# Performance work log

Measured on AMD Instinct MI355X. Metric: run time of the kernel, lower is better.

## Reference

```python
import jax, jax.numpy as jnp
import numpy as np

NUM_USERS = 100000
NUM_ITEMS = 50000
N = NUM_USERS + NUM_ITEMS  # total nodes
DIM = 64                   # dim_h
E = 2000000                # number of edges
NUM_LAYERS = 2


def setup_inputs() -> dict:
    key = jax.random.key(0)
    k0, k1, k2, k3, k4 = jax.random.split(key, 5)
    edge_index = jax.random.randint(k0, (2, E), 0, N, dtype=jnp.int64)
    edge_weight = jax.random.uniform(k1, (E,), dtype=jnp.float32)
    # nn.init.normal_(std=0.01) embeddings
    emb_users = 0.01 * jax.random.normal(k2, (NUM_USERS, DIM), dtype=jnp.float32)
    emb_items = 0.01 * jax.random.normal(k3, (NUM_ITEMS, DIM), dtype=jnp.float32)
    # nn.Linear(dim_h, dim_h)
    kW, kb = jax.random.split(k4)
    bound = 1.0 / np.sqrt(DIM)
    W = jax.random.uniform(kW, (DIM, DIM), minval=-bound, maxval=bound, dtype=jnp.float32)
    b = jax.random.uniform(kb, (DIM,), minval=-bound, maxval=bound, dtype=jnp.float32)
    return {"edge_index": edge_index, "edge_weight": edge_weight,
            "emb_users": emb_users, "emb_items": emb_items, "W": W, "b": b}


def reference(edge_index, edge_weight, emb_users, emb_items, W, b):
    # emb = cat([user_emb, item_emb])  -> [N, DIM]
    emb = jnp.concatenate([emb_users, emb_items], axis=0)
    src, dst = edge_index[0], edge_index[1]
    acc = emb  # running sum over layer embeddings (embs list)
    for _ in range(NUM_LAYERS):
        # LGConv with edge_weight: out[i] = sum_{j->i} w * x[j], then .relu()
        msg = edge_weight[:, None] * emb[src]            # [E, DIM] gather
        emb = jax.nn.relu(jax.ops.segment_sum(msg, dst, num_segments=N))
        acc = acc + emb
    emb_final = acc / (NUM_LAYERS + 1)                   # mean over stacked embs
    emb_final = emb_final @ W.T + b                      # final linear
    emb_users_final = emb_final[:NUM_USERS]
    emb_items_final = emb_final[NUM_USERS:]
    return (emb_users_final, emb_users, emb_items_final, emb_items)
```

## Files before the change

### kernel.cpp

```cpp
#include <hip/hip_runtime.h>
#include <hip/hip_fp16.h>

#define NUSERS 100000
#define NITEMS 50000
#define NNODES (NUSERS + NITEMS)
#define DIM 64
#define NEDGE 2000000
#define FT_ROWS 256
#define FT_BLOCKS ((NNODES + FT_ROWS - 1) / FT_ROWS)

#define BSH 7
#define NB ((NNODES + 127) >> BSH)
#define CAP 2048
#define CHUNK 4096
#define ABLOCKS ((NEDGE + CHUNK - 1) / CHUNK)
#define CONVB ((NNODES * DIM / 4 + 511) / 512)

__global__ __launch_bounds__(512)
void bucketconv_kernel(const int* __restrict__ eidx, const float* __restrict__ ew,
                       int* __restrict__ gcur, int2* __restrict__ regions,
                       const float* __restrict__ eu, const float* __restrict__ eit,
                       __half* __restrict__ tbl) {
    const int t = threadIdx.x;

    if (blockIdx.x >= ABLOCKS) {
        long i = (long)(blockIdx.x - ABLOCKS) * 512 + t;
        const long total = (long)NNODES * DIM / 4;
        if (i < total) {
            const long ue = (long)NUSERS * DIM / 4;
            float4 v = (i < ue) ? ((const float4*)eu)[i] : ((const float4*)eit)[i - ue];
            ((__half2*)tbl)[2 * i + 0] = __floats2half2_rn(v.x, v.y);
            ((__half2*)tbl)[2 * i + 1] = __floats2half2_rn(v.z, v.w);
        }
        return;
    }

    __shared__ int cursor_s[NB];
    __shared__ int excl_s[NB];
    __shared__ int gbase_s[NB];
    __shared__ int scanbuf[512];
    __shared__ int2 stage[CHUNK];
    __shared__ unsigned short sbkt[CHUNK];

    const int e0 = blockIdx.x * CHUNK;
    const int cnt_edges = min(CHUNK, NEDGE - e0);

    for (int i = t; i < NB; i += 512) cursor_s[i] = 0;
    __syncthreads();

    int2 recs[8];
    int bk[8];
    const int e4base = e0 >> 2;
#pragma unroll
    for (int k = 0; k < 2; ++k) {
        int g = k * 512 + t;
        bool ok = (4 * g) < cnt_edges;
        int4 s4 = make_int4(0, 0, 0, 0), d4 = make_int4(0, 0, 0, 0);
        float4 w4 = make_float4(0.f, 0.f, 0.f, 0.f);
        if (ok) {
            int e4 = e4base + g;
            s4 = ((const int4*)eidx)[e4];
            d4 = ((const int4*)eidx)[(NEDGE >> 2) + e4];
            w4 = ((const float4*)ew)[e4];
        }
        int ss[4] = {s4.x, s4.y, s4.z, s4.w};
        int dd[4] = {d4.x, d4.y, d4.z, d4.w};
        float ww[4] = {w4.x, w4.y, w4.z, w4.w};
#pragma unroll
        for (int j = 0; j < 4; ++j) {
            int idx = 4 * k + j;
            if (ok) {
                int d = dd[j];
                int b = d >> BSH;
                bk[idx] = b;
                recs[idx].x = ss[j] | ((d & 127) << 18);
                recs[idx].y = __float_as_int(ww[j]);
                atomicAdd(&cursor_s[b], 1);
            } else {
                bk[idx] = -1;
            }
        }
    }
    __syncthreads();

    int myv[3];
    int tsum = 0;
    const int base_i = t * 3;
#pragma unroll
    for (int j = 0; j < 3; ++j) {
        int i = base_i + j;
        myv[j] = (i < NB) ? cursor_s[i] : 0;
        tsum += myv[j];
    }
    scanbuf[t] = tsum;
    __syncthreads();
    for (int d = 1; d < 512; d <<= 1) {
        int u = (t >= d) ? scanbuf[t - d] : 0;
        __syncthreads();
        scanbuf[t] += u;
        __syncthreads();
    }
    int run = scanbuf[t] - tsum;
#pragma unroll
    for (int j = 0; j < 3; ++j) {
        int i = base_i + j;
        if (i < NB) {
            excl_s[i] = run;
            cursor_s[i] = run;
            if (myv[j] > 0) gbase_s[i] = atomicAdd(&gcur[i], myv[j]);
            run += myv[j];
        }
    }
    __syncthreads();

#pragma unroll
    for (int k = 0; k < 8; ++k) {
        if (bk[k] >= 0) {
            int p = atomicAdd(&cursor_s[bk[k]], 1);
            stage[p] = recs[k];
            sbkt[p] = (unsigned short)bk[k];
        }
    }
    __syncthreads();

    for (int i = t; i < cnt_edges; i += 512) {
        int b = sbkt[i];
        int gpos = gbase_s[b] + (i - excl_s[b]);
        if (gpos < CAP) regions[(long)b * CAP + gpos] = stage[i];
    }
}

__global__ __launch_bounds__(512)
void sortpull1_kernel(const int* __restrict__ gcur, const int2* __restrict__ regions,
                      const __half* __restrict__ tbl,
                      int2* __restrict__ edge_sorted, int2* __restrict__ rs,
                      __half* __restrict__ buf1h) {
    __shared__ int2 srec[CAP];
    __shared__ int cnt[128];
    __shared__ int excl[128];
    __shared__ int scanbuf[128];
    const int t = threadIdx.x;
    const int b = blockIdx.x;
    const int node0 = b << BSH;
    const int ecnt = min(gcur[b], CAP);
    const long gbase = (long)b * CAP;

    if (t < 128) cnt[t] = 0;
    __syncthreads();

    int2 recs[4];
#pragma unroll
    for (int k = 0; k < 4; ++k) {
        int i = k * 512 + t;
        if (i < ecnt) {
            recs[k] = regions[gbase + i];
            atomicAdd(&cnt[(recs[k].x >> 18) & 127], 1);
        }
    }
    __syncthreads();

    if (t < 128) scanbuf[t] = cnt[t];
    __syncthreads();
    for (int d = 1; d < 128; d <<= 1) {
        int u = 0;
        if (t < 128 && t >= d) u = scanbuf[t - d];
        __syncthreads();
        if (t < 128) scanbuf[t] += u;
        __syncthreads();
    }
    if (t < 128) {
        excl[t] = scanbuf[t] - cnt[t];
        cnt[t] = scanbuf[t] - cnt[t];
    }
    __syncthreads();

#pragma unroll
    for (int k = 0; k < 4; ++k) {
        int i = k * 512 + t;
        if (i < ecnt) {
            int d = (recs[k].x >> 18) & 127;
            int p = atomicAdd(&cnt[d], 1);
            int2 o;
            o.x = recs[k].x & 0x3FFFF;
            o.y = recs[k].y;
            srec[p] = o;
        }
    }
    __syncthreads();

    for (int i = t; i < ecnt; i += 512) edge_sorted[gbase + i] = srec[i];
    if (t < 128) {
        int node = node0 + t;
        if (node < NNODES) {
            int2 p;
            p.x = (int)gbase + excl[t];
            p.y = (int)gbase + cnt[t];
            rs[node] = p;
        }
    }

    const int lane = t & 63;
    const int wv = t >> 6;
    const int half = lane >> 5;
    const int hl = lane & 31;
    const __half2* tb2 = (const __half2*)tbl;
#pragma unroll 1
    for (int j = 0; j < 16; ++j) {
        const int local = wv * 16 + j;
        const int node = node0 + local;
        if (node >= NNODES) break;
        int i = excl[local];
        const int iend = cnt[local];
        float ax = 0.f, ay = 0.f, bx = 0.f, by = 0.f;
        for (; i + 7 < iend; i += 8) {
#pragma unroll
            for (int u = 0; u < 4; ++u) {
                int2 r = srec[i + 2 * u + half];
                float w = __int_as_float(r.y);
                float2 v = __half22float2(tb2[((long)r.x << 5) + hl]);
                if (u & 1) { bx = fmaf(w, v.x, bx); by = fmaf(w, v.y, by); }
                else       { ax = fmaf(w, v.x, ax); ay = fmaf(w, v.y, ay); }
            }
        }
        if (i < iend) {
#pragma unroll
            for (int u = 0; u < 4; ++u) {
                int idx = i + 2 * u + half;
                if (idx < iend) {
                    int2 r = srec[idx];
                    float w = __int_as_float(r.y);
                    float2 v = __half22float2(tb2[((long)r.x << 5) + hl]);
                    if (u & 1) { bx = fmaf(w, v.x, bx); by = fmaf(w, v.y, by); }
                    else       { ax = fmaf(w, v.x, ax); ay = fmaf(w, v.y, ay); }
                }
            }
        }
        float sx = ax + bx, sy = ay + by;
        sx += __shfl_xor(sx, 32);
        sy += __shfl_xor(sy, 32);
        if (half == 0) {
            ((__half2*)buf1h)[((long)node << 5) + hl] =
                __floats2half2_rn(fmaxf(sx, 0.f), fmaxf(sy, 0.f));
        }
    }
}

__global__ __launch_bounds__(512)
void pull2_kernel(const int* __restrict__ gcur, const int2* __restrict__ rs,
                  const int2* __restrict__ edge_sorted,
                  const __half* __restrict__ in_emb,
                  __half* __restrict__ out_emb) {
    __shared__ int2 srec[CAP];
    __shared__ int2 rsl[128];
    const int t = threadIdx.x;
    const int b = blockIdx.x;
    const int node0 = b << BSH;
    const int ecnt = min(gcur[b], CAP);
    const long gbase = (long)b * CAP;

    for (int i = t; i < ecnt; i += 512) srec[i] = edge_sorted[gbase + i];
    if (t < 128) {
        int node = node0 + t;
        rsl[t] = (node < NNODES) ? rs[node] : make_int2(0, 0);
    }
    __syncthreads();

    const int lane = t & 63;
    const int wv = t >> 6;
    const int half = lane >> 5;
    const int hl = lane & 31;
    const __half2* tb2 = (const __half2*)in_emb;
#pragma unroll 1
    for (int j = 0; j < 16; ++j) {
        const int local = wv * 16 + j;
        const int node = node0 + local;
        if (node >= NNODES) break;
        int i = rsl[local].x - (int)gbase;
        const int iend = rsl[local].y - (int)gbase;
        float ax = 0.f, ay = 0.f, bx = 0.f, by = 0.f;
        for (; i + 7 < iend; i += 8) {
#pragma unroll
            for (int u = 0; u < 4; ++u) {
                int2 r = srec[i + 2 * u + half];
                float w = __int_as_float(r.y);
                float2 v = __half22float2(tb2[((long)r.x << 5) + hl]);
                if (u & 1) { bx = fmaf(w, v.x, bx); by = fmaf(w, v.y, by); }
                else       { ax = fmaf(w, v.x, ax); ay = fmaf(w, v.y, ay); }
            }
        }
        if (i < iend) {
#pragma unroll
            for (int u = 0; u < 4; ++u) {
                int idx = i + 2 * u + half;
                if (idx < iend) {
                    int2 r = srec[idx];
                    float w = __int_as_float(r.y);
                    float2 v = __half22float2(tb2[((long)r.x << 5) + hl]);
                    if (u & 1) { bx = fmaf(w, v.x, bx); by = fmaf(w, v.y, by); }
                    else       { ax = fmaf(w, v.x, ax); ay = fmaf(w, v.y, ay); }
                }
            }
        }
        float sx = ax + bx, sy = ay + by;
        sx += __shfl_xor(sx, 32);
        sy += __shfl_xor(sy, 32);
        if (half == 0) {
            ((__half2*)out_emb)[((long)node << 5) + hl] =
                __floats2half2_rn(fmaxf(sx, 0.f), fmaxf(sy, 0.f));
        }
    }
}

__global__ __launch_bounds__(512)
void final_kernel(const float* __restrict__ eu, const float* __restrict__ eit,
                  const __half* __restrict__ e1, const __half* __restrict__ e2,
                  const float* __restrict__ W, const float* __restrict__ bias,
                  float* __restrict__ out) {
    __shared__ float4 As4[FT_ROWS * 16];
    __shared__ float Wt[64][64];
    const int t = threadIdx.x;
    const int lane = t & 63;
    const int wv = t >> 6;
    const long R0 = (long)blockIdx.x * FT_ROWS;

#pragma unroll
    for (int it = 0; it < 2; ++it) {
        int idx = it * 512 + t;
        int j = idx >> 4, q = idx & 15;
        float4 w = ((const float4*)W)[idx];
        Wt[4 * q + 0][j] = w.x; Wt[4 * q + 1][j] = w.y;
        Wt[4 * q + 2][j] = w.z; Wt[4 * q + 3][j] = w.w;
    }

#pragma unroll
    for (int it = 0; it < 8; ++it) {
        int idx = it * 512 + t;
        long row = R0 + (idx >> 4);
        if (row < NNODES) {
            int q = idx & 15;
            const float4* g0;
            long co;
            if (row < NUSERS) {
                g0 = (const float4*)(eu + (row << 6));
                co = (long)NUSERS * DIM + (row << 6);
            } else {
                g0 = (const float4*)(eit + ((row - NUSERS) << 6));
                co = (long)2 * NUSERS * DIM + (long)NITEMS * DIM + ((row - NUSERS) << 6);
            }
            float4 v0 = g0[q];
            ((float4*)(out + co))[q] = v0;
            const __half2* h1 = (const __half2*)(e1 + (row << 6));
            const __half2* h2 = (const __half2*)(e2 + (row << 6));
            float2 f1a = __half22float2(h1[2 * q]), f1b = __half22float2(h1[2 * q + 1]);
            float2 f2a = __half22float2(h2[2 * q]), f2b = __half22float2(h2[2 * q + 1]);
            float4 s;
            s.x = v0.x + f1a.x + f2a.x; s.y = v0.y + f1a.y + f2a.y;
            s.z = v0.z + f1b.x + f2b.x; s.w = v0.w + f1b.y + f2b.y;
            As4[idx] = s;
        }
    }
    __syncthreads();

    float wreg[64];
#pragma unroll
    for (int k = 0; k < 64; ++k) wreg[k] = Wt[k][lane];
    const float bj = bias[lane];

#pragma unroll 4
    for (int r = 0; r < 32; ++r) {
        int tr = wv * 32 + r;
        long row = R0 + tr;
        if (row >= NNODES) break;
        const float4* a = As4 + tr * 16;
        float s0 = 0.f, s1 = 0.f;
#pragma unroll
        for (int k = 0; k < 16; ++k) {
            float4 v = a[k];
            s0 = fmaf(v.x, wreg[4 * k + 0], s0);
            s1 = fmaf(v.y, wreg[4 * k + 1], s1);
            s0 = fmaf(v.z, wreg[4 * k + 2], s0);
            s1 = fmaf(v.w, wreg[4 * k + 3], s1);
        }
        float val = fmaf(s0 + s1, (1.0f / 3.0f), bj);
        long o = (row < NUSERS) ? row * DIM
                                : (long)2 * NUSERS * DIM + (row - NUSERS) * DIM;
        out[o + lane] = val;
    }
}

extern "C" void kernel_launch(void* const* d_in, const int* in_sizes, int n_in,
                              void* d_out, int out_size, void* d_ws, size_t ws_size,
                              hipStream_t stream) {
    const int*   eidx = (const int*)d_in[0];
    const float* ew   = (const float*)d_in[1];
    const float* eu   = (const float*)d_in[2];
    const float* eit  = (const float*)d_in[3];
    const float* W    = (const float*)d_in[4];
    const float* bias = (const float*)d_in[5];
    float* out = (float*)d_out;

    const size_t nfeat = (size_t)NNODES * DIM;
    __half* tbl         = (__half*)d_ws;
    __half* buf1h       = tbl + nfeat;
    __half* buf2h       = buf1h + nfeat;
    int2*   regions     = (int2*)(buf2h + nfeat);
    int2*   edge_sorted = regions + (long)NB * CAP;
    int2*   rs          = edge_sorted + (long)NB * CAP;
    int*    gcur        = (int*)(rs + NNODES);

    hipMemsetAsync(gcur, 0, NB * sizeof(int), stream);

    bucketconv_kernel<<<ABLOCKS + CONVB, 512, 0, stream>>>(eidx, ew, gcur, regions,
                                                           eu, eit, tbl);

    sortpull1_kernel<<<NB, 512, 0, stream>>>(gcur, regions, tbl,
                                             edge_sorted, rs, buf1h);

    pull2_kernel<<<NB, 512, 0, stream>>>(gcur, rs, edge_sorted, buf1h, buf2h);

    final_kernel<<<FT_BLOCKS, 512, 0, stream>>>(eu, eit, buf1h, buf2h, W, bias, out);
}
```

Baseline: 347.5 us.

## Fuse layer-mean accumulation into pull2 and simplify final linear kernel

```diff
diff --git a/kernel.cpp b/kernel.cpp
--- a/kernel.cpp
+++ b/kernel.cpp
@@ -248,8 +248,9 @@
 __global__ __launch_bounds__(512)
 void pull2_kernel(const int* __restrict__ gcur, const int2* __restrict__ rs,
                   const int2* __restrict__ edge_sorted,
-                  const __half* __restrict__ in_emb,
-                  __half* __restrict__ out_emb) {
+                  const __half* __restrict__ buf1h,
+                  const float* __restrict__ eu, const float* __restrict__ eit,
+                  float* __restrict__ xbuf) {
     __shared__ int2 srec[CAP];
     __shared__ int2 rsl[128];
     const int t = threadIdx.x;
@@ -269,7 +270,7 @@
     const int wv = t >> 6;
     const int half = lane >> 5;
     const int hl = lane & 31;
-    const __half2* tb2 = (const __half2*)in_emb;
+    const __half2* tb2 = (const __half2*)buf1h;
 #pragma unroll 1
     for (int j = 0; j < 16; ++j) {
         const int local = wv * 16 + j;
@@ -305,19 +306,25 @@
         sx += __shfl_xor(sx, 32);
         sy += __shfl_xor(sy, 32);
         if (half == 0) {
-            ((__half2*)out_emb)[((long)node << 5) + hl] =
-                __floats2half2_rn(fmaxf(sx, 0.f), fmaxf(sy, 0.f));
+            const float2* e0p = (node < NUSERS)
+                ? (const float2*)(eu + ((long)node << 6))
+                : (const float2*)(eit + ((long)(node - NUSERS) << 6));
+            float2 e0v = e0p[hl];
+            float2 e1v = __half22float2(((const __half2*)buf1h)[((long)node << 5) + hl]);
+            float2 xo;
+            xo.x = (e0v.x + e1v.x + fmaxf(sx, 0.f)) * (1.0f / 3.0f);
+            xo.y = (e0v.y + e1v.y + fmaxf(sy, 0.f)) * (1.0f / 3.0f);
+            ((float2*)xbuf)[((long)node << 5) + hl] = xo;
         }
     }
 }
 
 __global__ __launch_bounds__(512)
 void final_kernel(const float* __restrict__ eu, const float* __restrict__ eit,
-                  const __half* __restrict__ e1, const __half* __restrict__ e2,
+                  const float* __restrict__ xbuf,
                   const float* __restrict__ W, const float* __restrict__ bias,
                   float* __restrict__ out) {
-    __shared__ float4 As4[FT_ROWS * 16];
-    __shared__ float Wt[64][64];
+    __shared__ float Wt[64][65];
     const int t = threadIdx.x;
     const int lane = t & 63;
     const int wv = t >> 6;
@@ -332,31 +339,23 @@
         Wt[4 * q + 2][j] = w.z; Wt[4 * q + 3][j] = w.w;
     }
 
-#pragma unroll
-    for (int it = 0; it < 8; ++it) {
-        int idx = it * 512 + t;
-        long row = R0 + (idx >> 4);
-        if (row < NNODES) {
-            int q = idx & 15;
-            const float4* g0;
-            long co;
-            if (row < NUSERS) {
-                g0 = (const float4*)(eu + (row << 6));
-                co = (long)NUSERS * DIM + (row << 6);
-            } else {
-                g0 = (const float4*)(eit + ((row - NUSERS) << 6));
-                co = (long)2 * NUSERS * DIM + (long)NITEMS * DIM + ((row - NUSERS) << 6);
-            }
-            float4 v0 = g0[q];
-            ((float4*)(out + co))[q] = v0;
-            const __half2* h1 = (const __half2*)(e1 + (row << 6));
-            const __half2* h2 = (const __half2*)(e2 + (row << 6));
-            float2 f1a = __half22float2(h1[2 * q]), f1b = __half22float2(h1[2 * q + 1]);
-            float2 f2a = __half22float2(h2[2 * q]), f2b = __half22float2(h2[2 * q + 1]);
-            float4 s;
-            s.x = v0.x + f1a.x + f2a.x; s.y = v0.y + f1a.y + f2a.y;
-            s.z = v0.z + f1b.x + f2b.x; s.w = v0.w + f1b.y + f2b.y;
-            As4[idx] = s;
+    {
+        const float4* geu = (const float4*)eu;
+        const float4* geit = (const float4*)eit;
+        float4* oc_u = (float4*)(out + (long)NUSERS * DIM);
+        float4* oc_i = (float4*)(out + (long)2 * NUSERS * DIM + (long)NITEMS * DIM);
+#pragma unroll
+        for (int it = 0; it < 8; ++it) {
+            long idx = R0 * 16 + it * 512 + t;
+            long row = idx >> 4;
+            if (row < NNODES) {
+                if (row < NUSERS) {
+                    oc_u[idx] = geu[idx];
+                } else {
+                    long idx2 = idx - (long)NUSERS * 16;
+                    oc_i[idx2] = geit[idx2];
+                }
+            }
         }
     }
     __syncthreads();
@@ -366,25 +365,18 @@
     for (int k = 0; k < 64; ++k) wreg[k] = Wt[k][lane];
     const float bj = bias[lane];
 
-#pragma unroll 4
+#pragma unroll 1
     for (int r = 0; r < 32; ++r) {
-        int tr = wv * 32 + r;
-        long row = R0 + tr;
+        long row = R0 + wv * 32 + r;
         if (row >= NNODES) break;
-        const float4* a = As4 + tr * 16;
-        float s0 = 0.f, s1 = 0.f;
-#pragma unroll
-        for (int k = 0; k < 16; ++k) {
-            float4 v = a[k];
-            s0 = fmaf(v.x, wreg[4 * k + 0], s0);
-            s1 = fmaf(v.y, wreg[4 * k + 1], s1);
-            s0 = fmaf(v.z, wreg[4 * k + 2], s0);
-            s1 = fmaf(v.w, wreg[4 * k + 3], s1);
-        }
-        float val = fmaf(s0 + s1, (1.0f / 3.0f), bj);
+        int urow = __builtin_amdgcn_readfirstlane((int)row);
+        const float* xr = xbuf + ((long)urow << 6);
+        float acc = bj;
+#pragma unroll
+        for (int k = 0; k < 64; ++k) acc = fmaf(xr[k], wreg[k], acc);
         long o = (row < NUSERS) ? row * DIM
                                 : (long)2 * NUSERS * DIM + (row - NUSERS) * DIM;
-        out[o + lane] = val;
+        out[o + lane] = acc;
     }
 }
 
@@ -402,8 +394,8 @@
     const size_t nfeat = (size_t)NNODES * DIM;
     __half* tbl         = (__half*)d_ws;
     __half* buf1h       = tbl + nfeat;
-    __half* buf2h       = buf1h + nfeat;
-    int2*   regions     = (int2*)(buf2h + nfeat);
+    float*  xbuf        = (float*)(buf1h + nfeat);
+    int2*   regions     = (int2*)(xbuf + nfeat);
     int2*   edge_sorted = regions + (long)NB * CAP;
     int2*   rs          = edge_sorted + (long)NB * CAP;
     int*    gcur        = (int*)(rs + NNODES);
@@ -416,7 +408,8 @@
     sortpull1_kernel<<<NB, 512, 0, stream>>>(gcur, regions, tbl,
                                              edge_sorted, rs, buf1h);
 
-    pull2_kernel<<<NB, 512, 0, stream>>>(gcur, rs, edge_sorted, buf1h, buf2h);
-
-    final_kernel<<<FT_BLOCKS, 512, 0, stream>>>(eu, eit, buf1h, buf2h, W, bias, out);
+    pull2_kernel<<<NB, 512, 0, stream>>>(gcur, rs, edge_sorted, buf1h,
+                                         eu, eit, xbuf);
+
+    final_kernel<<<FT_BLOCKS, 512, 0, stream>>>(eu, eit, xbuf, W, bias, out);
 }
```

Result: no change. 350.3 us (+0.8%).
